# Kernel optimization log

Hardware: AMD Instinct MI355X
Metric: run time of the kernel (lower is better)

Reference implementation:

```python
import jax, jax.numpy as jnp
from jax import lax
import numpy as np

VOCAB, EMBED, HIDDEN, BATCH, MAXLEN = 32000, 512, 1024, 64, 64


def setup_inputs() -> dict:
    key = jax.random.key(0)
    ks = jax.random.split(key, 18)
    s = 0.02
    H, E, V = HIDDEN, EMBED, VOCAB
    return {
        "thought": jax.random.normal(ks[0], (BATCH, H), jnp.float32),
        "emb_table": jax.random.normal(ks[1], (V, E), jnp.float32) * s,
        "w_ih0": jax.random.normal(ks[2], (4 * H, E + H), jnp.float32) * s,
        "w_hh0": jax.random.normal(ks[3], (4 * H, H), jnp.float32) * s,
        "b_ih0": jax.random.normal(ks[4], (4 * H,), jnp.float32) * s,
        "b_hh0": jax.random.normal(ks[5], (4 * H,), jnp.float32) * s,
        "w_ih1": jax.random.normal(ks[6], (4 * H, H), jnp.float32) * s,
        "w_hh1": jax.random.normal(ks[7], (4 * H, H), jnp.float32) * s,
        "b_ih1": jax.random.normal(ks[8], (4 * H,), jnp.float32) * s,
        "b_hh1": jax.random.normal(ks[9], (4 * H,), jnp.float32) * s,
        "gw1": jax.random.normal(ks[10], (H, H), jnp.float32) * s,
        "gb1": jax.random.normal(ks[11], (H,), jnp.float32) * s,
        "gw2": jax.random.normal(ks[12], (1, H), jnp.float32) * s,
        "gb2": jax.random.normal(ks[13], (1,), jnp.float32) * s,
        "out_w": jax.random.normal(ks[14], (V, H), jnp.float32) * s,
        "out_b": jax.random.normal(ks[15], (V,), jnp.float32) * s,
        "max_len": MAXLEN,
    }


def lstm_cell(x, h, c, w_ih, w_hh, b_ih, b_hh):
    # torch nn.LSTM gate order: i, f, g, o
    g = x @ w_ih.T + b_ih + h @ w_hh.T + b_hh
    i, f, gg, o = jnp.split(g, 4, axis=-1)
    c2 = jax.nn.sigmoid(f) * c + jax.nn.sigmoid(i) * jnp.tanh(gg)
    return jax.nn.sigmoid(o) * jnp.tanh(c2), c2


def reference(thought, emb_table, w_ih0, w_hh0, b_ih0, b_hh0, w_ih1, w_hh1,
              b_ih1, b_hh1, gw1, gb1, gw2, gb2, out_w, out_b, max_len):
    """Generation branch of BioDecoder.forward (captions=None), eval mode, epoch=0."""
    B, H = thought.shape
    V = out_w.shape[0]
    temperature, top_p, top_k = 0.9, 0.88, 60
    key = jax.random.key(42)
    rows = jnp.arange(B)[:, None]

    def filt(logits):
        # top-k filter
        kth = lax.top_k(logits, top_k)[0][:, -1:]
        logits = jnp.where(logits < kth, -jnp.inf, logits)
        # nucleus (top-p) filter
        sl, si = lax.top_k(logits, V)  # full descending sort
        cum = jnp.cumsum(jax.nn.softmax(sl, axis=-1), axis=-1)
        rm = cum > top_p
        rm = jnp.concatenate([jnp.zeros_like(rm[:, :1]), rm[:, :-1]], axis=-1)  # always keep best
        mask = jnp.zeros_like(rm).at[rows, si].set(rm)
        return jnp.where(mask, -jnp.inf, logits)

    def step(carry, t):
        h1, c1, h2, c2, prev_ctx, word, counts, hist = carry
        x = jnp.concatenate([emb_table[word], prev_ctx], axis=-1)  # [B, E+H]
        h1, c1 = lstm_cell(x, h1, c1, w_ih0, w_hh0, b_ih0, b_hh0)
        h2, c2 = lstm_cell(h1, h2, c2, w_ih1, w_hh1, b_ih1, b_hh1)
        gate = jax.nn.sigmoid(jnp.tanh(h2 @ gw1.T + gb1) @ gw2.T + gb2)  # [B,1]
        out = h2 * gate
        logits = out @ out_w.T + out_b  # [B, V]
        # recency-decayed repetition penalty over full generated history
        ar = jnp.arange(hist.shape[0])
        w = jnp.where(ar < t, 2.5 * jnp.power(0.8, jnp.maximum(t - ar, 0).astype(jnp.float32)), 0.0)
        pen = jnp.zeros((B, V), logits.dtype).at[rows, hist.T].add(
            jnp.broadcast_to(w[None, :], (B, hist.shape[0])))
        # global count penalty (token_counts shared across batch, as in source)
        logits = logits - pen - jnp.where(counts > 1, 2.0 * counts, 0.0)[None, :]
        logits = logits / temperature + (0.3 / (counts + 1.0))[None, :]
        logits = filt(logits)
        nxt = jax.random.categorical(jax.random.fold_in(key, t), logits, axis=-1)  # [B]
        counts = counts.at[nxt].add(1.0)
        hist = hist.at[t].set(nxt)
        return (h1, c1, h2, c2, out, nxt, counts, hist), nxt

    zeros_h = jnp.zeros_like(thought)
    carry0 = (thought, zeros_h, thought, zeros_h, thought,
              jnp.full((B,), 1, jnp.int32),
              jnp.zeros((V,), jnp.float32),
              jnp.zeros((max_len, B), jnp.int32))
    _, tokens = lax.scan(step, carry0, jnp.arange(max_len))
    return tokens.T  # [B, max_len]
```

## Files before the change

### kernel.cpp

```cpp
#include <hip/hip_runtime.h>
#include <stdint.h>
#include <math.h>

#pragma clang fp contract(off)

#define BATCH 64
#define HID   1024
#define EMBD  512
#define VOC   32000
#define G4    4096
#define MAXT  64
#define NTOPK 60
#define CAND_MAX 256

__device__ __forceinline__ float xla_tanh(float x) {
  float ax = fabsf(x);
  float xc = fminf(fmaxf(x, -9.0f), 9.0f);
  float x2 = xc * xc;
  float num = -2.76076847742355e-16f;
  num = fmaf(x2, num, 2.00018790482477e-13f);
  num = fmaf(x2, num, -8.60467152213735e-11f);
  num = fmaf(x2, num, 5.12229709037114e-08f);
  num = fmaf(x2, num, 1.48572235717979e-05f);
  num = fmaf(x2, num, 6.37261928875436e-04f);
  num = fmaf(x2, num, 4.89352455891786e-03f);
  num = xc * num;
  float den = 1.19825839466702e-06f;
  den = fmaf(x2, den, 1.18534705686654e-04f);
  den = fmaf(x2, den, 2.26843463243900e-03f);
  den = fmaf(x2, den, 4.89352518554385e-03f);
  float r = num / den;
  return (ax < 0.0004f) ? x : r;
}

__device__ __forceinline__ float xla_sigmoid(float x) {
  return 0.5f * xla_tanh(0.5f * x) + 0.5f;
}

__device__ __forceinline__ float cephes_expf(float _x) {
  float x = fminf(_x, 88.723164f);
  x = fmaxf(x, -88.723164f);
  float m = floorf(fmaf(x, 1.44269504088896341f, 0.5f));
  float r = fmaf(m, -0.693359375f, x);
  r = fmaf(m, 2.12194440e-4f, r);
  float r2 = r * r;
  float r3 = r2 * r;
  float y, y1, y2;
  y  = fmaf(1.9875691500E-4f, r, 1.3981999507E-3f);
  y1 = fmaf(4.1665795894E-2f, r, 1.6666665459E-1f);
  y2 = r + 1.0f;
  y  = fmaf(y, r, 8.3334519073E-3f);
  y1 = fmaf(y1, r, 5.0000001201E-1f);
  y  = fmaf(y, r3, y1);
  y  = fmaf(y, r2, y2);
  float res = ldexpf(y, (int)m);
  return fmaxf(res, _x);
}

__device__ __forceinline__ float cephes_logf(float _x) {
  float x = fmaxf(_x, 1.17549435e-38f);
  unsigned ux = __float_as_uint(x);
  int e_int = (int)(ux >> 23) - 126;
  x = __uint_as_float((ux & 0x007FFFFFu) | 0x3F000000u);
  float e = (float)e_int;
  if (x < 0.707106781186547524f) { e -= 1.0f; x = x + x - 1.0f; }
  else { x = x - 1.0f; }
  float z = x * x;
  float y = 7.0376836292E-2f;
  y = fmaf(y, x, -1.1514610310E-1f);
  y = fmaf(y, x,  1.1676998740E-1f);
  y = fmaf(y, x, -1.2420140846E-1f);
  y = fmaf(y, x,  1.4249322787E-1f);
  y = fmaf(y, x, -1.6668057665E-1f);
  y = fmaf(y, x,  2.0000714765E-1f);
  y = fmaf(y, x, -2.4999993993E-1f);
  y = fmaf(y, x,  3.3333331174E-1f);
  y = y * x;
  y = y * z;
  y = fmaf(e, -2.12194440e-4f, y);
  y = fmaf(-0.5f, z, y);
  float r = x + y;
  r = fmaf(e, 0.693359375f, r);
  return r;
}

__device__ __forceinline__ unsigned rotl32(unsigned v, int s) {
  return (v << s) | (v >> (32 - s));
}
__device__ __forceinline__ void threefry(unsigned k0, unsigned k1,
                                         unsigned& x0, unsigned& x1) {
  unsigned k2 = k0 ^ k1 ^ 0x1BD11BDAu;
  x0 += k0; x1 += k1;
  x0 += x1; x1 = rotl32(x1, 13); x1 ^= x0;
  x0 += x1; x1 = rotl32(x1, 15); x1 ^= x0;
  x0 += x1; x1 = rotl32(x1, 26); x1 ^= x0;
  x0 += x1; x1 = rotl32(x1,  6); x1 ^= x0;
  x0 += k1; x1 += k2 + 1u;
  x0 += x1; x1 = rotl32(x1, 17); x1 ^= x0;
  x0 += x1; x1 = rotl32(x1, 29); x1 ^= x0;
  x0 += x1; x1 = rotl32(x1, 16); x1 ^= x0;
  x0 += x1; x1 = rotl32(x1, 24); x1 ^= x0;
  x0 += k2; x1 += k0 + 2u;
  x0 += x1; x1 = rotl32(x1, 13); x1 ^= x0;
  x0 += x1; x1 = rotl32(x1, 15); x1 ^= x0;
  x0 += x1; x1 = rotl32(x1, 26); x1 ^= x0;
  x0 += x1; x1 = rotl32(x1,  6); x1 ^= x0;
  x0 += k0; x1 += k1 + 3u;
  x0 += x1; x1 = rotl32(x1, 17); x1 ^= x0;
  x0 += x1; x1 = rotl32(x1, 29); x1 ^= x0;
  x0 += x1; x1 = rotl32(x1, 16); x1 ^= x0;
  x0 += x1; x1 = rotl32(x1, 24); x1 ^= x0;
  x0 += k1; x1 += k2 + 4u;
  x0 += x1; x1 = rotl32(x1, 13); x1 ^= x0;
  x0 += x1; x1 = rotl32(x1, 15); x1 ^= x0;
  x0 += x1; x1 = rotl32(x1, 26); x1 ^= x0;
  x0 += x1; x1 = rotl32(x1,  6); x1 ^= x0;
  x0 += k2; x1 += k0 + 5u;
}

__device__ __forceinline__ float gumbel_val(unsigned k0, unsigned k1, int b, int v) {
  unsigned x0 = 0u, x1 = (unsigned)(b * VOC + v);
  threefry(k0, k1, x0, x1);
  unsigned bits = x0 ^ x1;
  float u = __uint_as_float(0x3f800000u | (bits >> 9)) - 1.0f;
  if (u == 0.0f) u = 1.17549435e-38f;
  return -cephes_logf(-cephes_logf(u));
}

__device__ __forceinline__ unsigned okey(float f) {
  unsigned u = __float_as_uint(f);
  return (u & 0x80000000u) ? ~u : (u | 0x80000000u);
}
__device__ __forceinline__ float okey_inv(unsigned key) {
  unsigned u = (key & 0x80000000u) ? (key & 0x7FFFFFFFu) : ~key;
  return __uint_as_float(u);
}

__global__ __launch_bounds__(256) void k_init(const float* __restrict__ thought,
    float* h1, float* c1, float* h2, float* c2, float* prev_ctx,
    float* counts, int* word, int* hist) {
  int i = blockIdx.x * blockDim.x + threadIdx.x;
  if (i < BATCH * HID) {
    float tv = thought[i];
    h1[i] = tv; h2[i] = tv; prev_ctx[i] = tv;
    c1[i] = 0.f; c2[i] = 0.f;
  }
  if (i < VOC) counts[i] = 0.f;
  if (i < BATCH) word[i] = 1;
  if (i < MAXT * BATCH) hist[i] = 0;
}

__global__ __launch_bounds__(256) void k_gates0(const float* __restrict__ emb,
    const int* __restrict__ word, const float* __restrict__ prev_ctx,
    const float* __restrict__ h1, const float* __restrict__ w_ih,
    const float* __restrict__ b_ih, const float* __restrict__ w_hh,
    const float* __restrict__ b_hh, float* __restrict__ g) {
  int jl = threadIdx.x & 7, bg = threadIdx.x >> 3;
  int j = blockIdx.x * 8 + jl;
  const float4* wi4 = (const float4*)(w_ih + (size_t)j * (EMBD + HID));
  const float4* wh4 = (const float4*)(w_hh + (size_t)j * HID);
  const float4* e4[2]; const float4* p4[2]; const float4* h4[2];
  #pragma unroll
  for (int i = 0; i < 2; ++i) {
    int b = bg + 32 * i;
    e4[i] = (const float4*)(emb + (size_t)word[b] * EMBD);
    p4[i] = (const float4*)(prev_ctx + (size_t)b * HID);
    h4[i] = (const float4*)(h1 + (size_t)b * HID);
  }
  float acc[2] = {0.f, 0.f};
  float shh[2] = {0.f, 0.f};
  for (int k = 0; k < EMBD / 4; ++k) {
    float4 w = wi4[k];
    #pragma unroll
    for (int i = 0; i < 2; ++i) {
      float4 a = e4[i][k];
      acc[i] = fmaf(a.x, w.x, acc[i]); acc[i] = fmaf(a.y, w.y, acc[i]);
      acc[i] = fmaf(a.z, w.z, acc[i]); acc[i] = fmaf(a.w, w.w, acc[i]);
    }
  }
  for (int k = 0; k < HID / 4; ++k) {
    float4 w = wi4[EMBD / 4 + k];
    #pragma unroll
    for (int i = 0; i < 2; ++i) {
      float4 a = p4[i][k];
      acc[i] = fmaf(a.x, w.x, acc[i]); acc[i] = fmaf(a.y, w.y, acc[i]);
      acc[i] = fmaf(a.z, w.z, acc[i]); acc[i] = fmaf(a.w, w.w, acc[i]);
    }
  }
  for (int k = 0; k < HID / 4; ++k) {
    float4 w = wh4[k];
    #pragma unroll
    for (int i = 0; i < 2; ++i) {
      float4 a = h4[i][k];
      shh[i] = fmaf(a.x, w.x, shh[i]); shh[i] = fmaf(a.y, w.y, shh[i]);
      shh[i] = fmaf(a.z, w.z, shh[i]); shh[i] = fmaf(a.w, w.w, shh[i]);
    }
  }
  float bi = b_ih[j], bh = b_hh[j];
  #pragma unroll
  for (int i = 0; i < 2; ++i) {
    int b = bg + 32 * i;
    g[(size_t)b * G4 + j] = ((acc[i] + bi) + shh[i]) + bh;
  }
}

__global__ __launch_bounds__(256) void k_gates1(const float* __restrict__ xin,
    const float* __restrict__ hin, const float* __restrict__ w_ih,
    const float* __restrict__ b_ih, const float* __restrict__ w_hh,
    const float* __restrict__ b_hh, float* __restrict__ g) {
  int jl = threadIdx.x & 7, bg = threadIdx.x >> 3;
  int j = blockIdx.x * 8 + jl;
  const float4* wi4 = (const float4*)(w_ih + (size_t)j * HID);
  const float4* wh4 = (const float4*)(w_hh + (size_t)j * HID);
  float acc[2] = {0.f, 0.f};
  float shh[2] = {0.f, 0.f};
  for (int k = 0; k < HID / 4; ++k) {
    float4 w = wi4[k];
    #pragma unroll
    for (int i = 0; i < 2; ++i) {
      float4 a = ((const float4*)(xin + (size_t)(bg + 32 * i) * HID))[k];
      acc[i] = fmaf(a.x, w.x, acc[i]); acc[i] = fmaf(a.y, w.y, acc[i]);
      acc[i] = fmaf(a.z, w.z, acc[i]); acc[i] = fmaf(a.w, w.w, acc[i]);
    }
  }
  for (int k = 0; k < HID / 4; ++k) {
    float4 w = wh4[k];
    #pragma unroll
    for (int i = 0; i < 2; ++i) {
      float4 a = ((const float4*)(hin + (size_t)(bg + 32 * i) * HID))[k];
      shh[i] = fmaf(a.x, w.x, shh[i]); shh[i] = fmaf(a.y, w.y, shh[i]);
      shh[i] = fmaf(a.z, w.z, shh[i]); shh[i] = fmaf(a.w, w.w, shh[i]);
    }
  }
  float bi = b_ih[j], bh = b_hh[j];
  #pragma unroll
  for (int i = 0; i < 2; ++i) {
    int b = bg + 32 * i;
    g[(size_t)b * G4 + j] = ((acc[i] + bi) + shh[i]) + bh;
  }
}

__global__ __launch_bounds__(256) void k_cell(const float* __restrict__ g,
    float* __restrict__ h, float* __restrict__ c) {
  int i = blockIdx.x * blockDim.x + threadIdx.x;
  int b = i >> 10, u = i & 1023;
  const float* gb = g + (size_t)b * G4;
  float iv = gb[u], fv = gb[u + 1024], gv = gb[u + 2048], ov = gb[u + 3072];
  float cold = c[i];
  float cnew = xla_sigmoid(fv) * cold + xla_sigmoid(iv) * xla_tanh(gv);
  float hnew = xla_sigmoid(ov) * xla_tanh(cnew);
  c[i] = cnew;
  h[i] = hnew;
}

__global__ __launch_bounds__(256) void k_gtmp(const float* __restrict__ h2,
    const float* __restrict__ gw1, const float* __restrict__ gb1,
    float* __restrict__ gtmp) {
  int ul = threadIdx.x & 3, b = threadIdx.x >> 2;
  int u = blockIdx.x * 4 + ul;
  const float4* w4 = (const float4*)(gw1 + (size_t)u * HID);
  const float4* a4 = (const float4*)(h2 + (size_t)b * HID);
  float acc = 0.f;
  for (int k = 0; k < HID / 4; ++k) {
    float4 w = w4[k];
    float4 a = a4[k];
    acc = fmaf(a.x, w.x, acc); acc = fmaf(a.y, w.y, acc);
    acc = fmaf(a.z, w.z, acc); acc = fmaf(a.w, w.w, acc);
  }
  gtmp[(size_t)b * HID + u] = xla_tanh(acc + gb1[u]);
}

__global__ __launch_bounds__(256) void k_gateout(const float* __restrict__ gtmp,
    const float* __restrict__ gw2, const float* __restrict__ gb2,
    const float* __restrict__ h2, float* __restrict__ prev_ctx) {
  int b = blockIdx.x, tid = threadIdx.x;
  __shared__ float red[256];
  __shared__ float gsh;
  float s = 0.f;
  for (int k = tid; k < HID; k += 256)
    s = fmaf(gtmp[(size_t)b * HID + k], gw2[k], s);
  red[tid] = s;
  __syncthreads();
  for (int st = 128; st > 0; st >>= 1) {
    if (tid < st) red[tid] += red[tid + st];
    __syncthreads();
  }
  if (tid == 0) gsh = xla_sigmoid(red[0] + gb2[0]);
  __syncthreads();
  float gate = gsh;
  for (int k = tid; k < HID; k += 256)
    prev_ctx[(size_t)b * HID + k] = h2[(size_t)b * HID + k] * gate;
}

__global__ __launch_bounds__(256) void k_logits(const float* __restrict__ outp,
    const float* __restrict__ out_w, const float* __restrict__ out_b,
    const float* __restrict__ counts, float* __restrict__ raw,
    float* __restrict__ adj) {
  __shared__ float act[16 * HID];
  int tid = threadIdx.x;
  int bbase = blockIdx.y * 16;
  const float4* src = (const float4*)(outp + (size_t)bbase * HID);
  float4* dst = (float4*)act;
  #pragma unroll
  for (int j = 0; j < 16; ++j) dst[tid + 256 * j] = src[tid + 256 * j];
  __syncthreads();
  int v = blockIdx.x * 256 + tid;
  const float4* w4 = (const float4*)(out_w + (size_t)v * HID);
  float acc[16];
  #pragma unroll
  for (int i = 0; i < 16; ++i) acc[i] = 0.f;
  for (int k = 0; k < HID / 4; ++k) {
    float4 w = w4[k];
    #pragma unroll
    for (int i = 0; i < 16; ++i) {
      float4 a = ((const float4*)(act + i * HID))[k];
      acc[i] = fmaf(a.x, w.x, acc[i]); acc[i] = fmaf(a.y, w.y, acc[i]);
      acc[i] = fmaf(a.z, w.z, acc[i]); acc[i] = fmaf(a.w, w.w, acc[i]);
    }
  }
  float c = counts[v];
  float cpen = (c > 1.0f) ? (2.0f * c) : 0.0f;
  float bonus = 0.3f / (c + 1.0f);
  float bv = out_b[v];
  #pragma unroll
  for (int i = 0; i < 16; ++i) {
    int b = bbase + i;
    float r = acc[i] + bv;
    raw[(size_t)b * VOC + v] = r;
    adj[(size_t)b * VOC + v] = (r - cpen) / 0.9f + bonus;
  }
}

__global__ __launch_bounds__(256) void k_sample(float* __restrict__ adj,
    const float* __restrict__ raw, float* __restrict__ counts,
    int* __restrict__ word, int* __restrict__ hist,
    int* __restrict__ out_tokens, int t) {
  int b = blockIdx.x, tid = threadIdx.x;
  float* row = adj + (size_t)b * VOC;
  __shared__ unsigned keys[VOC];
  __shared__ int wcnt[4];
  __shared__ int sh_cnt;
  __shared__ float cval[CAND_MAX];
  __shared__ int cidx[CAND_MAX];
  __shared__ float sval[CAND_MAX];
  __shared__ int sidx[CAND_MAX];
  __shared__ unsigned char kept[CAND_MAX];
  __shared__ float rval[256];
  __shared__ int ridx[256];
  __shared__ unsigned shk0, shk1;
  __shared__ int hcol[MAXT];
  __shared__ float wtab[MAXT];

  if (tid < t) hcol[tid] = hist[tid * BATCH + b];
  if (tid < MAXT) wtab[tid] = 2.5f * powf(0.8f, (float)tid);
  if (tid == 0) {
    sh_cnt = 0;
    unsigned a = 0u, cc = (unsigned)t;
    threefry(0u, 42u, a, cc);
    shk0 = a; shk1 = cc;
  }
  __syncthreads();

  if (tid < t) {
    int ar = tid;
    int tok = hcol[ar];
    bool first = true;
    for (int a2 = 0; a2 < ar; ++a2)
      if (hcol[a2] == tok) { first = false; break; }
    if (first) {
      float pen = 0.f;
      for (int a2 = ar; a2 < t; ++a2)
        if (hcol[a2] == tok) pen += wtab[t - a2];
      float c = counts[tok];
      float cpen = (c > 1.0f) ? (2.0f * c) : 0.0f;
      float bonus = 0.3f / (c + 1.0f);
      float r = raw[(size_t)b * VOC + tok];
      row[tok] = ((r - pen) - cpen) / 0.9f + bonus;
    }
  }
  __syncthreads();

  const float4* row4 = (const float4*)row;
  uint4* keys4 = (uint4*)keys;
  for (int i = tid; i < VOC / 4; i += 256) {
    float4 f = row4[i];
    uint4 kk;
    kk.x = okey(f.x); kk.y = okey(f.y); kk.z = okey(f.z); kk.w = okey(f.w);
    keys4[i] = kk;
  }
  __syncthreads();

  unsigned long long lo = 0ULL, hi = 1ULL << 32;
  for (int it = 0; it < 32; ++it) {
    unsigned mid = (unsigned)((lo + hi) >> 1);
    int cnt = 0;
    for (int i = tid; i < VOC; i += 256)
      cnt += (keys[i] >= mid) ? 1 : 0;
    #pragma unroll
    for (int off = 32; off > 0; off >>= 1)
      cnt += __shfl_xor(cnt, off, 64);
    if ((tid & 63) == 0) wcnt[tid >> 6] = cnt;
    __syncthreads();
    int total = wcnt[0] + wcnt[1] + wcnt[2] + wcnt[3];
    if (total >= NTOPK) lo = (unsigned long long)mid;
    else                hi = (unsigned long long)mid;
    __syncthreads();
  }
  unsigned kmin = (unsigned)lo;

  for (int v = tid; v < VOC; v += 256) {
    unsigned key = keys[v];
    if (key >= kmin) {
      int pos = atomicAdd(&sh_cnt, 1);
      if (pos < CAND_MAX) { cval[pos] = okey_inv(key); cidx[pos] = v; }
    }
  }
  __syncthreads();
  int C = sh_cnt; if (C > CAND_MAX) C = CAND_MAX;

  for (int i = tid; i < C; i += 256) {
    float vi = cval[i]; int ii = cidx[i]; int r = 0;
    for (int j = 0; j < C; ++j) {
      float vj = cval[j]; int ij = cidx[j];
      if (vj > vi || (vj == vi && ij < ii)) ++r;
    }
    sval[r] = vi; sidx[r] = ii;
  }
  __syncthreads();

  if (tid == 0) {
    float m = sval[0];
    float psum = 0.f;
    for (int j = 0; j < C; ++j) {
      float p = cephes_expf(sval[j] - m);
      cval[j] = p;
      psum += p;
    }
    float cum = 0.f;
    for (int j = 0; j < C; ++j) {
      kept[j] = (j == 0 || cum <= 0.88f) ? 1 : 0;
      cum += cval[j] / psum;
    }
  }
  __syncthreads();

  float bscore = -INFINITY; int bidx = 0x7FFFFFFF;
  for (int j = tid; j < C; j += 256) {
    if (kept[j]) {
      float gv = gumbel_val(shk0, shk1, b, sidx[j]);
      float sc = gv + sval[j];
      if (sc > bscore || (sc == bscore && sidx[j] < bidx)) { bscore = sc; bidx = sidx[j]; }
    }
  }
  rval[tid] = bscore; ridx[tid] = bidx;
  __syncthreads();
  for (int s = 128; s > 0; s >>= 1) {
    if (tid < s) {
      float ov = rval[tid + s]; int oi = ridx[tid + s];
      if (ov > rval[tid] || (ov == rval[tid] && oi < ridx[tid])) {
        rval[tid] = ov; ridx[tid] = oi;
      }
    }
    __syncthreads();
  }
  if (tid == 0) {
    int tok = ridx[0];
    word[b] = tok;
    hist[t * BATCH + b] = tok;
    out_tokens[b * MAXT + t] = tok;
    atomicAdd(&counts[tok], 1.0f);
  }
}

extern "C" void kernel_launch(void* const* d_in, const int* in_sizes, int n_in,
                              void* d_out, int out_size, void* d_ws, size_t ws_size,
                              hipStream_t stream) {
  const float* thought = (const float*)d_in[0];
  const float* emb     = (const float*)d_in[1];
  const float* w_ih0   = (const float*)d_in[2];
  const float* w_hh0   = (const float*)d_in[3];
  const float* b_ih0   = (const float*)d_in[4];
  const float* b_hh0   = (const float*)d_in[5];
  const float* w_ih1   = (const float*)d_in[6];
  const float* w_hh1   = (const float*)d_in[7];
  const float* b_ih1   = (const float*)d_in[8];
  const float* b_hh1   = (const float*)d_in[9];
  const float* gw1     = (const float*)d_in[10];
  const float* gb1     = (const float*)d_in[11];
  const float* gw2     = (const float*)d_in[12];
  const float* gb2     = (const float*)d_in[13];
  const float* out_w   = (const float*)d_in[14];
  const float* out_b   = (const float*)d_in[15];
  int* out_tokens = (int*)d_out;

  float* F = (float*)d_ws;
  float* h1       = F;
  float* c1       = F + 65536;
  float* h2       = F + 131072;
  float* c2       = F + 196608;
  float* prev_ctx = F + 262144;
  float* gtmp     = F + 327680;
  float* g0       = F + 393216;
  float* g1       = F + 655360;
  float* counts   = F + 917504;
  float* raw      = F + 949504;
  float* adj      = F + 2997504;
  int*   word     = (int*)(F + 5045504);
  int*   hist     = word + 64;

  k_init<<<256, 256, 0, stream>>>(thought, h1, c1, h2, c2, prev_ctx, counts, word, hist);
  for (int t = 0; t < MAXT; ++t) {
    k_gates0<<<512, 256, 0, stream>>>(emb, word, prev_ctx, h1, w_ih0, b_ih0, w_hh0, b_hh0, g0);
    k_cell<<<256, 256, 0, stream>>>(g0, h1, c1);
    k_gates1<<<512, 256, 0, stream>>>(h1, h2, w_ih1, b_ih1, w_hh1, b_hh1, g1);
    k_cell<<<256, 256, 0, stream>>>(g1, h2, c2);
    k_gtmp<<<256, 256, 0, stream>>>(h2, gw1, gb1, gtmp);
    k_gateout<<<64, 256, 0, stream>>>(gtmp, gw2, gb2, h2, prev_ctx);
    k_logits<<<dim3(125, 4), 256, 0, stream>>>(prev_ctx, out_w, out_b, counts, raw, adj);
    k_sample<<<64, 256, 0, stream>>>(adj, raw, counts, word, hist, out_tokens, t);
  }
}
```

Measured before the change: 41.51 ms.

## Fuse LSTM cell into gate GEMVs, retile logits kernel, vectorize top-k count

```diff
diff --git a/kernel.cpp b/kernel.cpp
--- a/kernel.cpp
+++ b/kernel.cpp
@@ -8,7 +8,6 @@
 #define HID   1024
 #define EMBD  512
 #define VOC   32000
-#define G4    4096
 #define MAXT  64
 #define NTOPK 60
 #define CAND_MAX 256
@@ -137,12 +136,12 @@
 }
 
 __global__ __launch_bounds__(256) void k_init(const float* __restrict__ thought,
-    float* h1, float* c1, float* h2, float* c2, float* prev_ctx,
+    float* h1a, float* h2a, float* c1, float* c2, float* prev_ctx,
     float* counts, int* word, int* hist) {
   int i = blockIdx.x * blockDim.x + threadIdx.x;
   if (i < BATCH * HID) {
     float tv = thought[i];
-    h1[i] = tv; h2[i] = tv; prev_ctx[i] = tv;
+    h1a[i] = tv; h2a[i] = tv; prev_ctx[i] = tv;
     c1[i] = 0.f; c2[i] = 0.f;
   }
   if (i < VOC) counts[i] = 0.f;
@@ -150,13 +149,17 @@
   if (i < MAXT * BATCH) hist[i] = 0;
 }
 
-__global__ __launch_bounds__(256) void k_gates0(const float* __restrict__ emb,
+__global__ __launch_bounds__(256) void k_gates0f(const float* __restrict__ emb,
     const int* __restrict__ word, const float* __restrict__ prev_ctx,
-    const float* __restrict__ h1, const float* __restrict__ w_ih,
+    const float* __restrict__ h1r, const float* __restrict__ w_ih,
     const float* __restrict__ b_ih, const float* __restrict__ w_hh,
-    const float* __restrict__ b_hh, float* __restrict__ g) {
+    const float* __restrict__ b_hh, float* __restrict__ h1w,
+    float* __restrict__ c1) {
   int jl = threadIdx.x & 7, bg = threadIdx.x >> 3;
-  int j = blockIdx.x * 8 + jl;
+  int gate = jl & 3, usel = jl >> 2;
+  int u = blockIdx.x * 2 + usel;
+  int j = gate * 1024 + u;
+  __shared__ float sg[2][4][64];
   const float4* wi4 = (const float4*)(w_ih + (size_t)j * (EMBD + HID));
   const float4* wh4 = (const float4*)(w_hh + (size_t)j * HID);
   const float4* e4[2]; const float4* p4[2]; const float4* h4[2];
@@ -165,7 +168,7 @@
     int b = bg + 32 * i;
     e4[i] = (const float4*)(emb + (size_t)word[b] * EMBD);
     p4[i] = (const float4*)(prev_ctx + (size_t)b * HID);
-    h4[i] = (const float4*)(h1 + (size_t)b * HID);
+    h4[i] = (const float4*)(h1r + (size_t)b * HID);
   }
   float acc[2] = {0.f, 0.f};
   float shh[2] = {0.f, 0.f};
@@ -200,16 +203,31 @@
   #pragma unroll
   for (int i = 0; i < 2; ++i) {
     int b = bg + 32 * i;
-    g[(size_t)b * G4 + j] = ((acc[i] + bi) + shh[i]) + bh;
-  }
-}
-
-__global__ __launch_bounds__(256) void k_gates1(const float* __restrict__ xin,
+    sg[usel][gate][b] = ((acc[i] + bi) + shh[i]) + bh;
+  }
+  __syncthreads();
+  if (threadIdx.x < 128) {
+    int us = threadIdx.x >> 6, b = threadIdx.x & 63;
+    int uu = blockIdx.x * 2 + us;
+    float iv = sg[us][0][b], fv = sg[us][1][b], gv = sg[us][2][b], ov = sg[us][3][b];
+    size_t idx = (size_t)b * HID + uu;
+    float cold = c1[idx];
+    float cnew = xla_sigmoid(fv) * cold + xla_sigmoid(iv) * xla_tanh(gv);
+    c1[idx] = cnew;
+    h1w[idx] = xla_sigmoid(ov) * xla_tanh(cnew);
+  }
+}
+
+__global__ __launch_bounds__(256) void k_gates1f(const float* __restrict__ xin,
     const float* __restrict__ hin, const float* __restrict__ w_ih,
     const float* __restrict__ b_ih, const float* __restrict__ w_hh,
-    const float* __restrict__ b_hh, float* __restrict__ g) {
+    const float* __restrict__ b_hh, float* __restrict__ h2w,
+    float* __restrict__ c2) {
   int jl = threadIdx.x & 7, bg = threadIdx.x >> 3;
-  int j = blockIdx.x * 8 + jl;
+  int gate = jl & 3, usel = jl >> 2;
+  int u = blockIdx.x * 2 + usel;
+  int j = gate * 1024 + u;
+  __shared__ float sg[2][4][64];
   const float4* wi4 = (const float4*)(w_ih + (size_t)j * HID);
   const float4* wh4 = (const float4*)(w_hh + (size_t)j * HID);
   float acc[2] = {0.f, 0.f};
@@ -236,21 +254,19 @@
   #pragma unroll
   for (int i = 0; i < 2; ++i) {
     int b = bg + 32 * i;
-    g[(size_t)b * G4 + j] = ((acc[i] + bi) + shh[i]) + bh;
-  }
-}
-
-__global__ __launch_bounds__(256) void k_cell(const float* __restrict__ g,
-    float* __restrict__ h, float* __restrict__ c) {
-  int i = blockIdx.x * blockDim.x + threadIdx.x;
-  int b = i >> 10, u = i & 1023;
-  const float* gb = g + (size_t)b * G4;
-  float iv = gb[u], fv = gb[u + 1024], gv = gb[u + 2048], ov = gb[u + 3072];
-  float cold = c[i];
-  float cnew = xla_sigmoid(fv) * cold + xla_sigmoid(iv) * xla_tanh(gv);
-  float hnew = xla_sigmoid(ov) * xla_tanh(cnew);
-  c[i] = cnew;
-  h[i] = hnew;
+    sg[usel][gate][b] = ((acc[i] + bi) + shh[i]) + bh;
+  }
+  __syncthreads();
+  if (threadIdx.x < 128) {
+    int us = threadIdx.x >> 6, b = threadIdx.x & 63;
+    int uu = blockIdx.x * 2 + us;
+    float iv = sg[us][0][b], fv = sg[us][1][b], gv = sg[us][2][b], ov = sg[us][3][b];
+    size_t idx = (size_t)b * HID + uu;
+    float cold = c2[idx];
+    float cnew = xla_sigmoid(fv) * cold + xla_sigmoid(iv) * xla_tanh(gv);
+    c2[idx] = cnew;
+    h2w[idx] = xla_sigmoid(ov) * xla_tanh(cnew);
+  }
 }
 
 __global__ __launch_bounds__(256) void k_gtmp(const float* __restrict__ h2,
@@ -296,38 +312,56 @@
     const float* __restrict__ out_w, const float* __restrict__ out_b,
     const float* __restrict__ counts, float* __restrict__ raw,
     float* __restrict__ adj) {
-  __shared__ float act[16 * HID];
-  int tid = threadIdx.x;
-  int bbase = blockIdx.y * 16;
-  const float4* src = (const float4*)(outp + (size_t)bbase * HID);
-  float4* dst = (float4*)act;
+  int lane = threadIdx.x & 63;
+  int wave = threadIdx.x >> 6;
+  int vbase = blockIdx.x * 1024 + wave * 256 + lane;
+  int bbase = blockIdx.y * 4;
+  const float4* ob4 = (const float4*)(outp + (size_t)bbase * HID);
+  const float4* wp[4];
   #pragma unroll
-  for (int j = 0; j < 16; ++j) dst[tid + 256 * j] = src[tid + 256 * j];
-  __syncthreads();
-  int v = blockIdx.x * 256 + tid;
-  const float4* w4 = (const float4*)(out_w + (size_t)v * HID);
-  float acc[16];
+  for (int vi = 0; vi < 4; ++vi) {
+    int v = vbase + 64 * vi; if (v > VOC - 1) v = VOC - 1;
+    wp[vi] = (const float4*)(out_w + (size_t)v * HID);
+  }
+  float acc[4][4];
   #pragma unroll
-  for (int i = 0; i < 16; ++i) acc[i] = 0.f;
+  for (int vi = 0; vi < 4; ++vi)
+    #pragma unroll
+    for (int bi = 0; bi < 4; ++bi) acc[vi][bi] = 0.f;
   for (int k = 0; k < HID / 4; ++k) {
-    float4 w = w4[k];
-    #pragma unroll
-    for (int i = 0; i < 16; ++i) {
-      float4 a = ((const float4*)(act + i * HID))[k];
-      acc[i] = fmaf(a.x, w.x, acc[i]); acc[i] = fmaf(a.y, w.y, acc[i]);
-      acc[i] = fmaf(a.z, w.z, acc[i]); acc[i] = fmaf(a.w, w.w, acc[i]);
-    }
-  }
-  float c = counts[v];
-  float cpen = (c > 1.0f) ? (2.0f * c) : 0.0f;
-  float bonus = 0.3f / (c + 1.0f);
-  float bv = out_b[v];
+    float4 a0 = ob4[k];
+    float4 a1 = ob4[k + 256];
+    float4 a2 = ob4[k + 512];
+    float4 a3 = ob4[k + 768];
+    #pragma unroll
+    for (int vi = 0; vi < 4; ++vi) {
+      float4 w = wp[vi][k];
+      acc[vi][0] = fmaf(a0.x, w.x, acc[vi][0]); acc[vi][0] = fmaf(a0.y, w.y, acc[vi][0]);
+      acc[vi][0] = fmaf(a0.z, w.z, acc[vi][0]); acc[vi][0] = fmaf(a0.w, w.w, acc[vi][0]);
+      acc[vi][1] = fmaf(a1.x, w.x, acc[vi][1]); acc[vi][1] = fmaf(a1.y, w.y, acc[vi][1]);
+      acc[vi][1] = fmaf(a1.z, w.z, acc[vi][1]); acc[vi][1] = fmaf(a1.w, w.w, acc[vi][1]);
+      acc[vi][2] = fmaf(a2.x, w.x, acc[vi][2]); acc[vi][2] = fmaf(a2.y, w.y, acc[vi][2]);
+      acc[vi][2] = fmaf(a2.z, w.z, acc[vi][2]); acc[vi][2] = fmaf(a2.w, w.w, acc[vi][2]);
+      acc[vi][3] = fmaf(a3.x, w.x, acc[vi][3]); acc[vi][3] = fmaf(a3.y, w.y, acc[vi][3]);
+      acc[vi][3] = fmaf(a3.z, w.z, acc[vi][3]); acc[vi][3] = fmaf(a3.w, w.w, acc[vi][3]);
+    }
+  }
   #pragma unroll
-  for (int i = 0; i < 16; ++i) {
-    int b = bbase + i;
-    float r = acc[i] + bv;
-    raw[(size_t)b * VOC + v] = r;
-    adj[(size_t)b * VOC + v] = (r - cpen) / 0.9f + bonus;
+  for (int vi = 0; vi < 4; ++vi) {
+    int v = vbase + 64 * vi;
+    if (v < VOC) {
+      float c = counts[v];
+      float cpen = (c > 1.0f) ? (2.0f * c) : 0.0f;
+      float bonus = 0.3f / (c + 1.0f);
+      float bv = out_b[v];
+      #pragma unroll
+      for (int bi = 0; bi < 4; ++bi) {
+        int b = bbase + bi;
+        float r = acc[vi][bi] + bv;
+        raw[(size_t)b * VOC + v] = r;
+        adj[(size_t)b * VOC + v] = (r - cpen) / 0.9f + bonus;
+      }
+    }
   }
 }
 
@@ -394,8 +428,13 @@
   for (int it = 0; it < 32; ++it) {
     unsigned mid = (unsigned)((lo + hi) >> 1);
     int cnt = 0;
-    for (int i = tid; i < VOC; i += 256)
-      cnt += (keys[i] >= mid) ? 1 : 0;
+    for (int i = tid; i < VOC / 4; i += 256) {
+      uint4 kk = keys4[i];
+      cnt += (kk.x >= mid) ? 1 : 0;
+      cnt += (kk.y >= mid) ? 1 : 0;
+      cnt += (kk.z >= mid) ? 1 : 0;
+      cnt += (kk.w >= mid) ? 1 : 0;
+    }
     #pragma unroll
     for (int off = 32; off > 0; off >>= 1)
       cnt += __shfl_xor(cnt, off, 64);
@@ -494,29 +533,31 @@
   int* out_tokens = (int*)d_out;
 
   float* F = (float*)d_ws;
-  float* h1       = F;
-  float* c1       = F + 65536;
-  float* h2       = F + 131072;
-  float* c2       = F + 196608;
-  float* prev_ctx = F + 262144;
-  float* gtmp     = F + 327680;
-  float* g0       = F + 393216;
-  float* g1       = F + 655360;
-  float* counts   = F + 917504;
-  float* raw      = F + 949504;
-  float* adj      = F + 2997504;
-  int*   word     = (int*)(F + 5045504);
+  float* h1a      = F;
+  float* h1b      = F + 65536;
+  float* h2a      = F + 131072;
+  float* h2b      = F + 196608;
+  float* c1       = F + 262144;
+  float* c2       = F + 327680;
+  float* prev_ctx = F + 393216;
+  float* gtmp     = F + 458752;
+  float* counts   = F + 524288;
+  float* raw      = F + 556288;
+  float* adj      = F + 2604288;
+  int*   word     = (int*)(F + 4652288);
   int*   hist     = word + 64;
 
-  k_init<<<256, 256, 0, stream>>>(thought, h1, c1, h2, c2, prev_ctx, counts, word, hist);
+  k_init<<<256, 256, 0, stream>>>(thought, h1a, h2a, c1, c2, prev_ctx, counts, word, hist);
   for (int t = 0; t < MAXT; ++t) {
-    k_gates0<<<512, 256, 0, stream>>>(emb, word, prev_ctx, h1, w_ih0, b_ih0, w_hh0, b_hh0, g0);
-    k_cell<<<256, 256, 0, stream>>>(g0, h1, c1);
-    k_gates1<<<512, 256, 0, stream>>>(h1, h2, w_ih1, b_ih1, w_hh1, b_hh1, g1);
-    k_cell<<<256, 256, 0, stream>>>(g1, h2, c2);
-    k_gtmp<<<256, 256, 0, stream>>>(h2, gw1, gb1, gtmp);
-    k_gateout<<<64, 256, 0, stream>>>(gtmp, gw2, gb2, h2, prev_ctx);
-    k_logits<<<dim3(125, 4), 256, 0, stream>>>(prev_ctx, out_w, out_b, counts, raw, adj);
+    const float* h1r = (t & 1) ? h1b : h1a;
+    float*       h1w = (t & 1) ? h1a : h1b;
+    const float* h2r = (t & 1) ? h2b : h2a;
+    float*       h2w = (t & 1) ? h2a : h2b;
+    k_gates0f<<<512, 256, 0, stream>>>(emb, word, prev_ctx, h1r, w_ih0, b_ih0, w_hh0, b_hh0, h1w, c1);
+    k_gates1f<<<512, 256, 0, stream>>>(h1w, h2r, w_ih1, b_ih1, w_hh1, b_hh1, h2w, c2);
+    k_gtmp<<<256, 256, 0, stream>>>(h2w, gw1, gb1, gtmp);
+    k_gateout<<<64, 256, 0, stream>>>(gtmp, gw2, gb2, h2w, prev_ctx);
+    k_logits<<<dim3(32, 16), 256, 0, stream>>>(prev_ctx, out_w, out_b, counts, raw, adj);
     k_sample<<<64, 256, 0, stream>>>(adj, raw, counts, word, hist, out_tokens, t);
   }
 }
```

Measured after the change: 57.41 ms. 1.38x slower.
